# Optimization experiments

Measured on AMD Instinct MI355X. Metric: run time of the kernel, lower is better.

The kernel has to match this reference:

```python
import jax, jax.numpy as jnp
import numpy as np

N_NODES = 10000


def setup_inputs() -> dict:
    key = jax.random.key(0)
    ks = jax.random.split(key, 12)
    B, N, H, D_IN, E = 8, N_NODES, 128, 256, 160000
    s = 0.05
    return {
        "x": jax.random.normal(ks[0], (B, D_IN), jnp.float32),
        "h_prev": jax.random.normal(ks[1], (B, N, H), jnp.float32),
        "src": jax.random.randint(ks[2], (E,), 0, N, jnp.int32),
        "dst": jax.random.randint(ks[3], (E,), 0, N, jnp.int32),
        "w_r": jax.random.normal(ks[4], (D_IN, H), jnp.float32) * s,
        "b_r": jax.random.normal(ks[5], (H,), jnp.float32) * s,
        "w_z": jax.random.normal(ks[6], (D_IN, H), jnp.float32) * s,
        "b_z": jax.random.normal(ks[7], (H,), jnp.float32) * s,
        "w_h": jax.random.normal(ks[8], (D_IN, H), jnp.float32) * s,
        "b_h": jax.random.normal(ks[9], (H,), jnp.float32) * s,
        "gcn_w": jax.random.normal(ks[10], (H, H), jnp.float32) * s,
        "gcn_b": jax.random.normal(ks[11], (H,), jnp.float32) * s,
    }


def _graph_conv(h, src, dst, gcn_w, gcn_b):
    """DGL GraphConv, norm='both': out = D_in^{-1/2} A D_out^{-1/2} h W + b.
    h: (B, N, H); same graph structure shared across the batch."""
    N = h.shape[1]
    ones = jnp.ones(src.shape, h.dtype)
    out_deg = jax.ops.segment_sum(ones, src, num_segments=N)
    in_deg = jax.ops.segment_sum(ones, dst, num_segments=N)
    norm_out = jnp.where(out_deg > 0, jax.lax.rsqrt(jnp.maximum(out_deg, 1.0)), 0.0)
    norm_in = jnp.where(in_deg > 0, jax.lax.rsqrt(jnp.maximum(in_deg, 1.0)), 0.0)
    hs = h * norm_out[None, :, None]            # (B, N, H)
    msg = hs[:, src, :]                          # (B, E, H) gather
    agg = jax.vmap(lambda m: jax.ops.segment_sum(m, dst, num_segments=N))(msg)
    agg = agg * norm_in[None, :, None]
    return jnp.einsum('bnh,hk->bnk', agg, gcn_w) + gcn_b


def reference(x, h_prev, src, dst, w_r, b_r, w_z, b_z, w_h, b_h, gcn_w, gcn_b):
    h_conv = _graph_conv(h_prev, src, dst, gcn_w, gcn_b)   # (B, N, H)
    x_r = (x @ w_r + b_r)[:, None, :]                      # (B, 1, H) broadcast over N
    x_z = (x @ w_z + b_z)[:, None, :]
    x_h = (x @ w_h + b_h)[:, None, :]
    r_t = jax.nn.sigmoid(x_r + h_conv)
    z_t = jax.nn.sigmoid(x_z + h_conv)
    h_tilde = jnp.tanh(x_h + r_t * h_conv)
    return (1.0 - z_t) * h_prev + z_t * h_tilde
```

## Files before the change

kernel.cpp:

```cpp
#include <hip/hip_runtime.h>
#include <hip/hip_bf16.h>

#define B_   8
#define N_   10000
#define H_   128
#define DIN_ 256
#define E_   160000
#define EPAD_ (E_ + 7 * N_ + 8)
#define ZBYTES_ (3 * N_ * 4 + EPAD_ * 8)

typedef unsigned int uint_;
typedef unsigned short ushort_;
typedef __attribute__((ext_vector_type(8))) short short8;
typedef __attribute__((ext_vector_type(4))) float f32x4;

__device__ __forceinline__ float sigmoidf_(float v) { return 1.f / (1.f + __expf(-v)); }
__device__ __forceinline__ float tanh_fast(float v) { float e = __expf(2.f * v); return 1.f - 2.f / (e + 1.f); }

__device__ __forceinline__ ushort_ f2bf(float f) {
    union { float f; uint_ u; } v; v.f = f;
    uint_ r = v.u + 0x7fff + ((v.u >> 16) & 1);
    return (ushort_)(r >> 16);
}
#define BF_LO(u) __uint_as_float((u) << 16)
#define BF_HI(u) __uint_as_float((u) & 0xffff0000u)

__global__ __launch_bounds__(256) void zero_k(uint4* __restrict__ p) {
    int i = blockIdx.x * 256 + threadIdx.x;
    if (i < ZBYTES_ / 16) p[i] = (uint4){0u, 0u, 0u, 0u};
}

__global__ __launch_bounds__(1024) void norms_scan_k(const int* __restrict__ out_deg, const int* __restrict__ in_deg,
                                                     float* __restrict__ norm_out, float* __restrict__ norm_in,
                                                     int* __restrict__ offsets) {
    __shared__ int buf[10240];
    __shared__ int part[1024];
    const int tid = threadIdx.x;
    #pragma unroll
    for (int q = 0; q < 10; ++q) {
        int idx = q * 1024 + tid;
        int d = (idx < N_) ? in_deg[idx] : 0;
        buf[idx] = (idx < N_) ? ((d + 7) & ~7) : 0;
        if (idx < N_) {
            int od = out_deg[idx];
            norm_out[idx] = od > 0 ? rsqrtf((float)od) : 0.f;
            norm_in[idx]  = d  > 0 ? rsqrtf((float)d)  : 0.f;
        }
    }
    __syncthreads();
    int local[10];
    int s = 0;
    #pragma unroll
    for (int q = 0; q < 10; ++q) {
        local[q] = s;
        s += buf[tid * 10 + q];
    }
    part[tid] = s;
    __syncthreads();
    for (int off = 1; off < 1024; off <<= 1) {
        int v = (tid >= off) ? part[tid - off] : 0;
        __syncthreads();
        part[tid] += v;
        __syncthreads();
    }
    int pre = (tid > 0) ? part[tid - 1] : 0;
    #pragma unroll
    for (int q = 0; q < 10; ++q)
        buf[tid * 10 + q] = pre + local[q];
    __syncthreads();
    #pragma unroll
    for (int q = 0; q < 10; ++q) {
        int idx = q * 1024 + tid;
        if (idx < N_) offsets[idx] = buf[idx];
    }
    if (tid == 1023) offsets[N_] = part[1023];
}

__global__ __launch_bounds__(256) void xdeg_k(const float* __restrict__ x,
                                              const float* __restrict__ w_r, const float* __restrict__ b_r,
                                              const float* __restrict__ w_z, const float* __restrict__ b_z,
                                              const float* __restrict__ w_h, const float* __restrict__ b_h,
                                              const float* __restrict__ gcn_w, ushort_* __restrict__ wt,
                                              float* __restrict__ xr, float* __restrict__ xz, float* __restrict__ xh,
                                              const int* __restrict__ src, const int* __restrict__ dst,
                                              int* __restrict__ out_deg, int* __restrict__ in_deg) {
    __shared__ float part[2][128];
    const int bid = blockIdx.x;
    if (bid >= 32) {
        int e = (bid - 32) * 256 + threadIdx.x;
        if (e < E_) {
            atomicAdd(&out_deg[src[e]], 1);
            atomicAdd(&in_deg[dst[e]], 1);
        }
        return;
    }
    const int g = bid & 3, b = bid >> 2;
    if (g == 3) {
        if (b != 0) return;
        const int t = threadIdx.x;
        const int n = t >> 1;
        const int kb = (t & 1) * 64;
        #pragma unroll
        for (int i = 0; i < 8; ++i) {
            int k = kb + i * 8;
            uint4 o;
            o.x = (uint_)f2bf(gcn_w[(k + 0) * H_ + n]) | ((uint_)f2bf(gcn_w[(k + 1) * H_ + n]) << 16);
            o.y = (uint_)f2bf(gcn_w[(k + 2) * H_ + n]) | ((uint_)f2bf(gcn_w[(k + 3) * H_ + n]) << 16);
            o.z = (uint_)f2bf(gcn_w[(k + 4) * H_ + n]) | ((uint_)f2bf(gcn_w[(k + 5) * H_ + n]) << 16);
            o.w = (uint_)f2bf(gcn_w[(k + 6) * H_ + n]) | ((uint_)f2bf(gcn_w[(k + 7) * H_ + n]) << 16);
            *(uint4*)(wt + n * H_ + k) = o;
        }
        return;
    }
    const float* __restrict__ w  = g == 0 ? w_r : (g == 1 ? w_z : w_h);
    const float* __restrict__ bs = g == 0 ? b_r : (g == 1 ? b_z : b_h);
    float* __restrict__ o        = g == 0 ? xr  : (g == 1 ? xz  : xh);
    const int k = threadIdx.x & 127, half = threadIdx.x >> 7;
    const float* xb = x + b * DIN_;
    float a = 0.f;
    #pragma unroll 8
    for (int d = half * 128; d < half * 128 + 128; ++d)
        a += xb[d] * w[d * H_ + k];
    part[half][k] = a;
    __syncthreads();
    if (half == 0) o[b * H_ + k] = a + part[1][k] + bs[k];
}

__device__ __forceinline__ void load_tile_(f32x4 (&st)[8], const float* __restrict__ h,
                                           size_t bslab, int t, int tid) {
    #pragma unroll
    for (int i = 0; i < 8; ++i) {
        int f4 = i * 256 + tid;
        int row = f4 >> 5;
        int col4 = (f4 & 31) * 4;
        f32x4 v = {0.f, 0.f, 0.f, 0.f};
        int nn = t * 64 + row;
        if (nn < N_) v = *(const f32x4*)&h[(bslab + nn) * (size_t)H_ + col4];
        st[i] = v;
    }
}

__global__ __launch_bounds__(256) void fillgemm_k(const int* __restrict__ src, const int* __restrict__ dst,
                                                  const int* __restrict__ offsets, int* __restrict__ cursor,
                                                  const float* __restrict__ norm_out, int2* __restrict__ csr_ed,
                                                  const float* __restrict__ h, const ushort_* __restrict__ wt,
                                                  ushort_* __restrict__ hw) {
    __shared__ ushort_ WT_s[H_ * H_];
    __shared__ ushort_ A_s[64 * H_];
    const int bid = blockIdx.x;
    const int tid = threadIdx.x;
    if (bid >= 632) {
        int e = (bid - 632) * 256 + tid;
        if (e < E_) {
            int d = dst[e];
            int s = src[e];
            int pos = offsets[d] + atomicAdd(&cursor[d], 1);
            csr_ed[pos] = make_int2(s, __float_as_int(norm_out[s]));
        }
        return;
    }
    const int b  = bid & 7;
    const int ty = bid >> 3;
    const size_t bslab = (size_t)b * N_;

    #pragma unroll
    for (int i = 0; i < 8; ++i) {
        int c = i * 256 + tid;
        int n = c >> 4;
        int kus = (c & 15) * 8;
        uint4 v = ((const uint4*)wt)[c];
        *(uint4*)&WT_s[n * H_ + (kus ^ ((n & 7) << 3))] = v;
    }

    const int l = tid & 63;
    const int w = tid >> 6;
    const int lr = l & 15;
    const int kg = (l >> 4) * 8;
    const int arow = w * 16 + lr;

    int t = ty;
    f32x4 st[8];
    load_tile_(st, h, bslab, t, tid);

    for (;;) {
        #pragma unroll
        for (int i = 0; i < 8; ++i) {
            int f4 = i * 256 + tid;
            int row = f4 >> 5;
            int col4 = (f4 & 31) * 4;
            uint2 p;
            p.x = (uint_)f2bf(st[i][0]) | ((uint_)f2bf(st[i][1]) << 16);
            p.y = (uint_)f2bf(st[i][2]) | ((uint_)f2bf(st[i][3]) << 16);
            *(uint2*)&A_s[row * H_ + (col4 ^ ((row & 7) << 3))] = p;
        }
        __syncthreads();

        const int tn = t + 79;
        const bool more = tn < 157;
        f32x4 nx[8];
        if (more) load_tile_(nx, h, bslab, tn, tid);

        f32x4 acc[8];
        #pragma unroll
        for (int nf = 0; nf < 8; ++nf) acc[nf] = (f32x4){0.f, 0.f, 0.f, 0.f};

        #pragma unroll
        for (int kk = 0; kk < 4; ++kk) {
            int kus = kk * 32 + kg;
            short8 av = *(const short8*)&A_s[arow * H_ + (kus ^ ((arow & 7) << 3))];
            #pragma unroll
            for (int nf = 0; nf < 8; ++nf) {
                int nrow = nf * 16 + lr;
                short8 bv = *(const short8*)&WT_s[nrow * H_ + (kus ^ ((nrow & 7) << 3))];
                acc[nf] = __builtin_amdgcn_mfma_f32_16x16x32_bf16(av, bv, acc[nf], 0, 0, 0);
            }
        }

        const int n0 = t * 64;
        const int wrow0 = w * 16 + (l >> 4) * 4;
        #pragma unroll
        for (int nf = 0; nf < 8; ++nf) {
            int col = nf * 16 + lr;
            #pragma unroll
            for (int r = 0; r < 4; ++r) {
                int row = wrow0 + r;
                A_s[row * H_ + (col ^ ((row & 7) << 3))] = f2bf(acc[nf][r]);
            }
        }
        {
            int row = w * 16 + (l >> 2);
            int c0 = (l & 3) * 32;
            int swz = (row & 7) << 3;
            if (n0 + row < N_) {
                uint4 o0 = *(const uint4*)&A_s[row * H_ + ((c0 +  0) ^ swz)];
                uint4 o1 = *(const uint4*)&A_s[row * H_ + ((c0 +  8) ^ swz)];
                uint4 o2 = *(const uint4*)&A_s[row * H_ + ((c0 + 16) ^ swz)];
                uint4 o3 = *(const uint4*)&A_s[row * H_ + ((c0 + 24) ^ swz)];
                uint4* dstp = (uint4*)(hw + (bslab + n0 + row) * (size_t)H_ + c0);
                dstp[0] = o0; dstp[1] = o1; dstp[2] = o2; dstp[3] = o3;
            }
        }
        if (!more) break;
        __syncthreads();
        #pragma unroll
        for (int i = 0; i < 8; ++i) st[i] = nx[i];
        t = tn;
    }
}

#define PROC2_(Q)                                                      \
    {                                                                  \
        int   s0_ = __builtin_amdgcn_readfirstlane((Q).x);             \
        float c0_ = __uint_as_float((uint_)(Q).y);                     \
        int   s1_ = __builtin_amdgcn_readfirstlane((Q).z);             \
        float c1_ = __uint_as_float((uint_)(Q).w);                     \
        uint2 u0_ = *(const uint2*)(hb + (size_t)s0_ * H_);            \
        uint2 u1_ = *(const uint2*)(hb + (size_t)s1_ * H_);            \
        a0 += c0_ * BF_LO(u0_.x); a1 += c0_ * BF_HI(u0_.x);            \
        a2 += c0_ * BF_LO(u0_.y); a3 += c0_ * BF_HI(u0_.y);            \
        a0 += c1_ * BF_LO(u1_.x); a1 += c1_ * BF_HI(u1_.x);            \
        a2 += c1_ * BF_LO(u1_.y); a3 += c1_ * BF_HI(u1_.y);            \
    }

__global__ __launch_bounds__(256) void agg_gru_k(const ushort_* __restrict__ hw, const int* __restrict__ offsets,
                                                 const float* __restrict__ norm_in,
                                                 const int2* __restrict__ csr_ed,
                                                 const float* __restrict__ gcn_b,
                                                 const float* __restrict__ xr, const float* __restrict__ xz,
                                                 const float* __restrict__ xh,
                                                 const float* __restrict__ h_prev, float* __restrict__ out) {
    const int lane = threadIdx.x & 63;
    const int wave = threadIdx.x >> 6;
    const int pr = blockIdx.x & 3;
    const int ng = blockIdx.x >> 2;
    const int n  = ng * 4 + wave;
    const int bsub = lane >> 5;
    const int b  = pr * 2 + bsub;
    const int cl = lane & 31;
    const int col = cl * 4;
    const int o  = __builtin_amdgcn_readfirstlane(offsets[n]);
    const int dc = __builtin_amdgcn_readfirstlane(offsets[n + 1]) - o;
    const int4* __restrict__ ed4 = (const int4*)(csr_ed + o);
    const ushort_* __restrict__ hb = hw + (size_t)b * (N_ * H_) + col;

    const float ni = norm_in[n];
    const size_t off = ((size_t)b * N_ + n) * H_ + col;
    float4 hp = *(const float4*)(h_prev + off);
    float4 gb = *(const float4*)(gcn_b + col);
    float4 vr = *(const float4*)(xr + b * H_ + col);
    float4 vz = *(const float4*)(xz + b * H_ + col);
    float4 vh = *(const float4*)(xh + b * H_ + col);

    float a0 = 0.f, a1 = 0.f, a2 = 0.f, a3 = 0.f;
    if (dc > 0) {
        const int m = dc >> 1;
        int4 q0 = ed4[0], q1 = ed4[1], q2 = ed4[2], q3 = ed4[3];
        for (int j = 4; j < m; j += 4) {
            int4 p0 = ed4[j + 0], p1 = ed4[j + 1], p2 = ed4[j + 2], p3 = ed4[j + 3];
            PROC2_(q0); PROC2_(q1); PROC2_(q2); PROC2_(q3);
            q0 = p0; q1 = p1; q2 = p2; q3 = p3;
        }
        PROC2_(q0); PROC2_(q1); PROC2_(q2); PROC2_(q3);
    }

    float4 wv;
    {
        float hc = a0 * ni + gb.x;
        float rr = sigmoidf_(vr.x + hc);
        float zz = sigmoidf_(vz.x + hc);
        float ht = tanh_fast(vh.x + rr * hc);
        wv.x = (1.f - zz) * hp.x + zz * ht;
    }
    {
        float hc = a1 * ni + gb.y;
        float rr = sigmoidf_(vr.y + hc);
        float zz = sigmoidf_(vz.y + hc);
        float ht = tanh_fast(vh.y + rr * hc);
        wv.y = (1.f - zz) * hp.y + zz * ht;
    }
    {
        float hc = a2 * ni + gb.z;
        float rr = sigmoidf_(vr.z + hc);
        float zz = sigmoidf_(vz.z + hc);
        float ht = tanh_fast(vh.z + rr * hc);
        wv.z = (1.f - zz) * hp.z + zz * ht;
    }
    {
        float hc = a3 * ni + gb.w;
        float rr = sigmoidf_(vr.w + hc);
        float zz = sigmoidf_(vz.w + hc);
        float ht = tanh_fast(vh.w + rr * hc);
        wv.w = (1.f - zz) * hp.w + zz * ht;
    }
    *(float4*)(out + off) = wv;
}

extern "C" void kernel_launch(void* const* d_in, const int* in_sizes, int n_in,
                              void* d_out, int out_size, void* d_ws, size_t ws_size,
                              hipStream_t stream) {
    (void)in_sizes; (void)n_in; (void)out_size; (void)ws_size;
    const float* x      = (const float*)d_in[0];
    const float* h_prev = (const float*)d_in[1];
    const int*   src    = (const int*)d_in[2];
    const int*   dst    = (const int*)d_in[3];
    const float* w_r    = (const float*)d_in[4];
    const float* b_r    = (const float*)d_in[5];
    const float* w_z    = (const float*)d_in[6];
    const float* b_z    = (const float*)d_in[7];
    const float* w_h    = (const float*)d_in[8];
    const float* b_h    = (const float*)d_in[9];
    const float* gcn_w  = (const float*)d_in[10];
    const float* gcn_b  = (const float*)d_in[11];
    float* out = (float*)d_out;

    ushort_* hw = (ushort_*)d_ws;
    int* wsi = (int*)(hw + (size_t)B_ * N_ * H_);
    int* out_deg   = wsi;
    int* in_deg    = wsi + N_;
    int* cursor    = wsi + 2 * N_;
    int2* csr_ed   = (int2*)(wsi + 3 * N_);
    int* offsets   = (int*)(csr_ed + EPAD_);
    float* norm_out = (float*)(offsets + N_ + 1);
    float* norm_in  = norm_out + N_;
    float* xr = norm_in + N_;
    float* xz = xr + B_ * H_;
    float* xh = xz + B_ * H_;
    ushort_* wt = (ushort_*)(xh + B_ * H_);

    zero_k<<<(ZBYTES_ / 16 + 255) / 256, 256, 0, stream>>>((uint4*)wsi);
    xdeg_k<<<32 + (E_ + 255) / 256, 256, 0, stream>>>(x, w_r, b_r, w_z, b_z, w_h, b_h,
                                                      gcn_w, wt, xr, xz, xh,
                                                      src, dst, out_deg, in_deg);
    norms_scan_k<<<1, 1024, 0, stream>>>(out_deg, in_deg, norm_out, norm_in, offsets);
    fillgemm_k<<<632 + (E_ + 255) / 256, 256, 0, stream>>>(src, dst, offsets, cursor, norm_out, csr_ed,
                                                           h_prev, wt, hw);
    agg_gru_k<<<(N_ / 4) * 4, 256, 0, stream>>>(hw, offsets, norm_in, csr_ed,
                                                gcn_b, xr, xz, xh, h_prev, out);
}
```

Before: 94.06 us.

## Overlap degree scan with bf16 GEMM block and split CSR fill into own kernel

The single-block norm/offset scan kernel is folded into the GEMM launch as an extra block (256 threads, 40 items each), so the serial scan runs concurrently with the h·W GEMM instead of as its own launch before it. The CSR fill that depended on the scan's offsets moves into a separate small kernel launched after. The launch count stays the same, and the scan now runs with fewer threads doing more serial work. The scan block may also become the critical path of the GEMM kernel.

```diff
diff --git a/kernel.cpp b/kernel.cpp
--- a/kernel.cpp
+++ b/kernel.cpp
@@ -28,52 +28,6 @@
 __global__ __launch_bounds__(256) void zero_k(uint4* __restrict__ p) {
     int i = blockIdx.x * 256 + threadIdx.x;
     if (i < ZBYTES_ / 16) p[i] = (uint4){0u, 0u, 0u, 0u};
-}
-
-__global__ __launch_bounds__(1024) void norms_scan_k(const int* __restrict__ out_deg, const int* __restrict__ in_deg,
-                                                     float* __restrict__ norm_out, float* __restrict__ norm_in,
-                                                     int* __restrict__ offsets) {
-    __shared__ int buf[10240];
-    __shared__ int part[1024];
-    const int tid = threadIdx.x;
-    #pragma unroll
-    for (int q = 0; q < 10; ++q) {
-        int idx = q * 1024 + tid;
-        int d = (idx < N_) ? in_deg[idx] : 0;
-        buf[idx] = (idx < N_) ? ((d + 7) & ~7) : 0;
-        if (idx < N_) {
-            int od = out_deg[idx];
-            norm_out[idx] = od > 0 ? rsqrtf((float)od) : 0.f;
-            norm_in[idx]  = d  > 0 ? rsqrtf((float)d)  : 0.f;
-        }
-    }
-    __syncthreads();
-    int local[10];
-    int s = 0;
-    #pragma unroll
-    for (int q = 0; q < 10; ++q) {
-        local[q] = s;
-        s += buf[tid * 10 + q];
-    }
-    part[tid] = s;
-    __syncthreads();
-    for (int off = 1; off < 1024; off <<= 1) {
-        int v = (tid >= off) ? part[tid - off] : 0;
-        __syncthreads();
-        part[tid] += v;
-        __syncthreads();
-    }
-    int pre = (tid > 0) ? part[tid - 1] : 0;
-    #pragma unroll
-    for (int q = 0; q < 10; ++q)
-        buf[tid * 10 + q] = pre + local[q];
-    __syncthreads();
-    #pragma unroll
-    for (int q = 0; q < 10; ++q) {
-        int idx = q * 1024 + tid;
-        if (idx < N_) offsets[idx] = buf[idx];
-    }
-    if (tid == 1023) offsets[N_] = part[1023];
 }
 
 __global__ __launch_bounds__(256) void xdeg_k(const float* __restrict__ x,
@@ -140,25 +94,57 @@
     }
 }
 
-__global__ __launch_bounds__(256) void fillgemm_k(const int* __restrict__ src, const int* __restrict__ dst,
-                                                  const int* __restrict__ offsets, int* __restrict__ cursor,
-                                                  const float* __restrict__ norm_out, int2* __restrict__ csr_ed,
-                                                  const float* __restrict__ h, const ushort_* __restrict__ wt,
-                                                  ushort_* __restrict__ hw) {
-    __shared__ ushort_ WT_s[H_ * H_];
-    __shared__ ushort_ A_s[64 * H_];
+__global__ __launch_bounds__(256) void gemmscan_k(const float* __restrict__ h, const ushort_* __restrict__ wt,
+                                                  ushort_* __restrict__ hw,
+                                                  const int* __restrict__ out_deg, const int* __restrict__ in_deg,
+                                                  float* __restrict__ norm_out, float* __restrict__ norm_in,
+                                                  int* __restrict__ offsets) {
+    __shared__ __align__(16) char smem_raw[49152];
     const int bid = blockIdx.x;
     const int tid = threadIdx.x;
-    if (bid >= 632) {
-        int e = (bid - 632) * 256 + tid;
-        if (e < E_) {
-            int d = dst[e];
-            int s = src[e];
-            int pos = offsets[d] + atomicAdd(&cursor[d], 1);
-            csr_ed[pos] = make_int2(s, __float_as_int(norm_out[s]));
-        }
+    if (bid == 632) {
+        int* buf  = (int*)smem_raw;
+        int* part = (int*)(smem_raw + 40960);
+        #pragma unroll
+        for (int q = 0; q < 40; ++q) {
+            int idx = q * 256 + tid;
+            int d = (idx < N_) ? in_deg[idx] : 0;
+            buf[idx] = (idx < N_) ? ((d + 7) & ~7) : 0;
+            if (idx < N_) {
+                int od = out_deg[idx];
+                norm_out[idx] = od > 0 ? rsqrtf((float)od) : 0.f;
+                norm_in[idx]  = d  > 0 ? rsqrtf((float)d)  : 0.f;
+            }
+        }
+        __syncthreads();
+        int base = tid * 40;
+        int s = 0;
+        for (int q = 0; q < 40; ++q) {
+            int v = buf[base + q];
+            buf[base + q] = s;
+            s += v;
+        }
+        part[tid] = s;
+        __syncthreads();
+        for (int off = 1; off < 256; off <<= 1) {
+            int v = (tid >= off) ? part[tid - off] : 0;
+            __syncthreads();
+            part[tid] += v;
+            __syncthreads();
+        }
+        int pre = (tid > 0) ? part[tid - 1] : 0;
+        for (int q = 0; q < 40; ++q) buf[base + q] += pre;
+        __syncthreads();
+        #pragma unroll
+        for (int q = 0; q < 40; ++q) {
+            int idx = q * 256 + tid;
+            if (idx < N_) offsets[idx] = buf[idx];
+        }
+        if (tid == 255) offsets[N_] = part[255];
         return;
     }
+    ushort_* WT_s = (ushort_*)smem_raw;
+    ushort_* A_s  = (ushort_*)smem_raw + H_ * H_;
     const int b  = bid & 7;
     const int ty = bid >> 3;
     const size_t bslab = (size_t)b * N_;
@@ -245,6 +231,19 @@
         #pragma unroll
         for (int i = 0; i < 8; ++i) st[i] = nx[i];
         t = tn;
+    }
+}
+
+__global__ __launch_bounds__(256) void fill_k(const int* __restrict__ src, const int* __restrict__ dst,
+                                              const int* __restrict__ offsets, int* __restrict__ cursor,
+                                              const float* __restrict__ norm_out,
+                                              int2* __restrict__ csr_ed) {
+    int e = blockIdx.x * 256 + threadIdx.x;
+    if (e < E_) {
+        int d = dst[e];
+        int s = src[e];
+        int pos = offsets[d] + atomicAdd(&cursor[d], 1);
+        csr_ed[pos] = make_int2(s, __float_as_int(norm_out[s]));
     }
 }
 
@@ -371,9 +370,9 @@
     xdeg_k<<<32 + (E_ + 255) / 256, 256, 0, stream>>>(x, w_r, b_r, w_z, b_z, w_h, b_h,
                                                       gcn_w, wt, xr, xz, xh,
                                                       src, dst, out_deg, in_deg);
-    norms_scan_k<<<1, 1024, 0, stream>>>(out_deg, in_deg, norm_out, norm_in, offsets);
-    fillgemm_k<<<632 + (E_ + 255) / 256, 256, 0, stream>>>(src, dst, offsets, cursor, norm_out, csr_ed,
-                                                           h_prev, wt, hw);
+    gemmscan_k<<<633, 256, 0, stream>>>(h_prev, wt, hw, out_deg, in_deg,
+                                        norm_out, norm_in, offsets);
+    fill_k<<<(E_ + 255) / 256, 256, 0, stream>>>(src, dst, offsets, cursor, norm_out, csr_ed);
     agg_gru_k<<<(N_ / 4) * 4, 256, 0, stream>>>(hw, offsets, norm_in, csr_ed,
                                                 gcn_b, xr, xz, xh, h_prev, out);
 }
```

Measured after the change: 98.98 us. 1.05x slower.
